# Optimization experiments

Measured on AMD Instinct MI355X. Metric: run time of the kernel, lower is better.

The kernel has to match this reference:

```python
import jax, jax.numpy as jnp
import numpy as np

B, T, C = 4, 2048, 1024
H, D = 16, 64          # n_head, head_size; H*D == C
FF = 4 * C             # compute_layer_scaling * n_embed
EPS = 1e-5


def layernorm(x, g, b):
    mu = jnp.mean(x, axis=-1, keepdims=True)
    var = jnp.var(x, axis=-1, keepdims=True)
    return (x - mu) * jax.lax.rsqrt(var + EPS) * g + b


def setup_inputs() -> dict:
    key = jax.random.key(0)
    ks = jax.random.split(key, 12)
    s_c = 1.0 / np.sqrt(C)
    s_ff = 1.0 / np.sqrt(FF)
    return {
        "x": jax.random.normal(ks[0], (B, T, C), dtype=jnp.float32),
        # per-head Q/K/V weights, stacked: [H, C, D] (Linear with bias=False)
        "Wq": jax.random.normal(ks[1], (H, C, D), dtype=jnp.float32) * s_c,
        "Wk": jax.random.normal(ks[2], (H, C, D), dtype=jnp.float32) * s_c,
        "Wv": jax.random.normal(ks[3], (H, C, D), dtype=jnp.float32) * s_c,
        "Wproj": jax.random.normal(ks[4], (C, C), dtype=jnp.float32) * s_c,
        "bproj": jnp.zeros((C,), dtype=jnp.float32),
        "W1": jax.random.normal(ks[5], (C, FF), dtype=jnp.float32) * s_c,
        "b1": jnp.zeros((FF,), dtype=jnp.float32),
        "W2": jax.random.normal(ks[6], (FF, FF), dtype=jnp.float32) * s_ff,
        "b2": jnp.zeros((FF,), dtype=jnp.float32),
        "W3": jax.random.normal(ks[7], (FF, C), dtype=jnp.float32) * s_ff,
        "b3": jnp.zeros((C,), dtype=jnp.float32),
        "ln1_g": jnp.ones((C,), dtype=jnp.float32),
        "ln1_b": jnp.zeros((C,), dtype=jnp.float32),
        "ln2_g": jnp.ones((C,), dtype=jnp.float32),
        "ln2_b": jnp.zeros((C,), dtype=jnp.float32),
    }


def reference(x, Wq, Wk, Wv, Wproj, bproj, W1, b1, W2, b2, W3, b3,
              ln1_g, ln1_b, ln2_g, ln2_b):
    # --- multi-head causal self-attention (pre-LN) ---
    h = layernorm(x, ln1_g, ln1_b)
    q = jnp.einsum("btc,hcd->bhtd", h, Wq)
    k = jnp.einsum("btc,hcd->bhtd", h, Wk)
    v = jnp.einsum("btc,hcd->bhtd", h, Wv)
    # NOTE: original scales by n_embed**-0.5 (C from x.shape), not head_size
    scores = jnp.einsum("bhtd,bhsd->bhts", q, k) * (C ** -0.5)
    causal = jnp.tril(jnp.ones((T, T), dtype=bool))
    scores = jnp.where(causal, scores, -jnp.inf)
    wei = jax.nn.softmax(scores, axis=-1)          # dropout p=0 -> identity
    attn = jnp.einsum("bhts,bhsd->bhtd", wei, v)
    attn = attn.transpose(0, 2, 1, 3).reshape(B, T, C)  # concat heads
    x = x + attn @ Wproj + bproj
    # --- feed-forward (pre-LN): C -> FF -> relu -> FF -> relu -> C ---
    h2 = layernorm(x, ln2_g, ln2_b)
    h2 = jax.nn.relu(h2 @ W1 + b1)
    h2 = jax.nn.relu(h2 @ W2 + b2)
    x = x + h2 @ W3 + b3
    return x
```

## Files before the change

kernel.cpp:

```cpp
#include <hip/hip_runtime.h>

typedef __bf16 bf16;
typedef bf16  bf16x8 __attribute__((ext_vector_type(8)));
typedef bf16  bf16x4 __attribute__((ext_vector_type(4)));
typedef float f32x4  __attribute__((ext_vector_type(4)));

#define T_SEQ 2048

__device__ __forceinline__ void gload_lds16(const bf16* g, bf16* l) {
    __builtin_amdgcn_global_load_lds(
        (const __attribute__((address_space(1))) unsigned int*)g,
        (__attribute__((address_space(3))) unsigned int*)l,
        16, 0, 0);
}

#define VMCNT(n) asm volatile("s_waitcnt vmcnt(" #n ")" ::: "memory")
#define BAR() do { asm volatile("" ::: "memory"); __builtin_amdgcn_s_barrier(); \
                   asm volatile("" ::: "memory"); } while (0)

__global__ __launch_bounds__(256) void transpose_f32_bf16(
    const float* __restrict__ in, bf16* __restrict__ out, int R, int Cc, int ldo)
{
    __shared__ float tile[32][33];
    const int bx = blockIdx.x * 32;
    const int by = blockIdx.y * 32;
    const long bi = (long)blockIdx.z * R * Cc;
    const long bo = (long)blockIdx.z * Cc * ldo;
    const int tx = threadIdx.x, ty = threadIdx.y;
#pragma unroll
    for (int i = 0; i < 4; ++i)
        tile[ty + i * 8][tx] = in[bi + (long)(by + ty + i * 8) * Cc + bx + tx];
    __syncthreads();
#pragma unroll
    for (int i = 0; i < 4; ++i)
        out[bo + (long)(bx + ty + i * 8) * ldo + by + tx] = (bf16)tile[tx][ty + i * 8];
}

__global__ __launch_bounds__(256) void transpose_bf16(
    const bf16* __restrict__ in, bf16* __restrict__ out, int ldi, int ldo)
{
    __shared__ bf16 tile[32][33];
    const int bx = blockIdx.x * 32;
    const int by = blockIdx.y * 32;
    const int tx = threadIdx.x, ty = threadIdx.y;
#pragma unroll
    for (int i = 0; i < 4; ++i)
        tile[ty + i * 8][tx] = in[(long)(by + ty + i * 8) * ldi + bx + tx];
    __syncthreads();
#pragma unroll
    for (int i = 0; i < 4; ++i)
        out[(long)(bx + ty + i * 8) * ldo + by + tx] = tile[tx][ty + i * 8];
}

__global__ __launch_bounds__(256) void ln_kernel(
    const float* __restrict__ x, const float* __restrict__ g,
    const float* __restrict__ bb, bf16* __restrict__ out)
{
    const long row = blockIdx.x;
    const int tid = threadIdx.x;
    const float4 v = ((const float4*)(x + row * 1024))[tid];
    float s  = v.x + v.y + v.z + v.w;
    float s2 = v.x * v.x + v.y * v.y + v.z * v.z + v.w * v.w;
#pragma unroll
    for (int off = 32; off >= 1; off >>= 1) {
        s  += __shfl_xor(s,  off, 64);
        s2 += __shfl_xor(s2, off, 64);
    }
    __shared__ float red[8];
    const int wid = tid >> 6;
    if ((tid & 63) == 0) { red[wid] = s; red[4 + wid] = s2; }
    __syncthreads();
    s  = red[0] + red[1] + red[2] + red[3];
    s2 = red[4] + red[5] + red[6] + red[7];
    const float mu   = s * (1.f / 1024.f);
    const float rstd = rsqrtf(s2 * (1.f / 1024.f) - mu * mu + 1e-5f);
    const float4 gv = ((const float4*)g)[tid];
    const float4 bv = ((const float4*)bb)[tid];
    bf16x4 ov;
    ov[0] = (bf16)((v.x - mu) * rstd * gv.x + bv.x);
    ov[1] = (bf16)((v.y - mu) * rstd * gv.y + bv.y);
    ov[2] = (bf16)((v.z - mu) * rstd * gv.z + bv.z);
    ov[3] = (bf16)((v.w - mu) * rstd * gv.w + bv.w);
    *(bf16x4*)(out + row * 1024 + tid * 4) = ov;
}

#define LOADA(BUFP, QM) do {                                                   \
    const char* ab_ = (BUFP) + (size_t)((wr * 64 + (QM) * 128 + fr) * 128);    \
    _Pragma("unroll") for (int m_ = 0; m_ < 4; ++m_) {                         \
        af[m_][0] = *(const bf16x8*)(ab_ + m_ * 2048 + so0);                   \
        af[m_][1] = *(const bf16x8*)(ab_ + m_ * 2048 + so1); } } while (0)

#define LOADB(BUFP, QN) do {                                                   \
    const char* bb_ = (BUFP) + (size_t)((wc * 32 + (QN) * 128 + fr) * 128);    \
    _Pragma("unroll") for (int n_ = 0; n_ < 2; ++n_) {                         \
        bfv[n_][0] = *(const bf16x8*)(bb_ + n_ * 2048 + so0);                  \
        bfv[n_][1] = *(const bf16x8*)(bb_ + n_ * 2048 + so1); } } while (0)

#define MMA(ACC) do { __builtin_amdgcn_s_setprio(1);                           \
    _Pragma("unroll") for (int m_ = 0; m_ < 4; ++m_)                           \
    _Pragma("unroll") for (int n_ = 0; n_ < 2; ++n_) {                         \
        ACC[m_][n_] = __builtin_amdgcn_mfma_f32_16x16x32_bf16(                 \
            af[m_][0], bfv[n_][0], ACC[m_][n_], 0, 0, 0);                      \
        ACC[m_][n_] = __builtin_amdgcn_mfma_f32_16x16x32_bf16(                 \
            af[m_][1], bfv[n_][1], ACC[m_][n_], 0, 0, 0); }                    \
    __builtin_amdgcn_s_setprio(0); } while (0)

#define TILE_BODY(PRE) do {                                                    \
    const char* abuf = cAs + ((size_t)cur << 15);                              \
    const char* bbuf = cBs + ((size_t)cur << 15);                              \
    const long kn = (long)(k + 1) * 64;                                        \
    LOADA(abuf, 0);                                                            \
    LOADB(bbuf, 0);                                                            \
    if (PRE) { stageA(nxt, 0, kn); stageB(nxt, 0, kn);                         \
               stageB(nxt, 1, kn); stageA(nxt, 1, kn); VMCNT(10); }            \
    else     { VMCNT(2); }                                                     \
    BAR(); MMA(a00); BAR();                                                    \
    LOADB(bbuf, 1);                                                            \
    if (PRE) { VMCNT(8); } else { VMCNT(0); }                                  \
    BAR(); MMA(a01); BAR();                                                    \
    LOADA(abuf, 1);                                                            \
    BAR(); MMA(a11); BAR();                                                    \
    LOADB(bbuf, 0);                                                            \
    if (PRE) { VMCNT(4); }                                                     \
    BAR(); MMA(a10); BAR(); } while (0)

template <int MODE>
__global__ __launch_bounds__(512, 2) void gemm256(
    const bf16* __restrict__ A, const bf16* __restrict__ Bt,
    const float* __restrict__ bias, const float* __restrict__ resid,
    void* __restrict__ outp, int M, int N, int K, int nbn)
{
    extern __shared__ __align__(16) char smem[];
    char* cAs = smem;
    char* cBs = smem + 65536;

    const int tid = threadIdx.x;
    const int wid = tid >> 6, lane = tid & 63;
    const int wr = wid >> 2, wc = wid & 3;
    const int fr = lane & 15, fq = lane >> 4;

    const int nwg = gridDim.x;
    const int cpx = nwg >> 3;
    const int b0  = blockIdx.x;
    const int bid = (b0 & 7) * cpx + (b0 >> 3);
    const long bm = bid / nbn, bn = bid % nbn;
    const long bmrow = bm * 256, bnrow = bn * 256;

    const int srow0 = wid * 8 + (lane >> 3);
    const int sslot = (lane & 7) ^ (lane >> 3);
    auto stageA = [&](int buf, int h, long kt) {
        const bf16* g = A + (size_t)(bmrow + h * 128 + srow0) * K + kt + sslot * 8;
        char* l = cAs + ((size_t)buf << 15) + h * 16384 + (size_t)wid * 1024;
        gload_lds16(g, (bf16*)l);
        gload_lds16(g + (size_t)64 * K, (bf16*)(l + 8192));
    };
    auto stageB = [&](int buf, int h, long kt) {
        const bf16* g = Bt + (size_t)(bnrow + h * 128 + srow0) * K + kt + sslot * 8;
        char* l = cBs + ((size_t)buf << 15) + h * 16384 + (size_t)wid * 1024;
        gload_lds16(g, (bf16*)l);
        gload_lds16(g + (size_t)64 * K, (bf16*)(l + 8192));
    };

    const int sx  = fr & 7;
    const int so0 = ((fq) ^ sx) * 16;
    const int so1 = ((4 + fq) ^ sx) * 16;

    bf16x8 af[4][2], bfv[2][2];
    f32x4 a00[4][2], a01[4][2], a11[4][2], a10[4][2];
#pragma unroll
    for (int m = 0; m < 4; ++m)
#pragma unroll
        for (int n = 0; n < 2; ++n) {
            a00[m][n] = {0.f, 0.f, 0.f, 0.f}; a01[m][n] = {0.f, 0.f, 0.f, 0.f};
            a11[m][n] = {0.f, 0.f, 0.f, 0.f}; a10[m][n] = {0.f, 0.f, 0.f, 0.f};
        }

    stageA(0, 0, 0); stageB(0, 0, 0); stageB(0, 1, 0); stageA(0, 1, 0);
    VMCNT(4);
    BAR();

    const int NT = K >> 6;
    int cur = 0, nxt = 1;
    int k = 0;
    for (; k < NT - 1; ++k) {
        cur = k & 1; nxt = cur ^ 1;
        TILE_BODY(true);
    }
    cur = k & 1; nxt = cur ^ 1;
    TILE_BODY(false);

    auto writeQ = [&](f32x4 (&acc)[4][2], int QM, int QN) {
#pragma unroll
        for (int m = 0; m < 4; ++m) {
            const long row0 = bmrow + wr * 64 + QM * 128 + m * 16 + fq * 4;
#pragma unroll
            for (int n = 0; n < 2; ++n) {
                const long col = bnrow + wc * 32 + QN * 128 + n * 16 + fr;
                const float bv = (MODE == 0) ? 0.f : bias[col];
#pragma unroll
                for (int j = 0; j < 4; ++j) {
                    const long row = row0 + j;
                    float v = acc[m][n][j] + bv;
                    if (MODE == 1) v = fmaxf(v, 0.f);
                    if (MODE == 2) {
                        v += resid[row * N + col];
                        ((float*)outp)[row * N + col] = v;
                    } else {
                        ((bf16*)outp)[row * N + col] = (bf16)v;
                    }
                }
            }
        }
    };
    writeQ(a00, 0, 0); writeQ(a01, 0, 1); writeQ(a11, 1, 1); writeQ(a10, 1, 0);
}

#define TILE_BODY_N(PRE, LAST) do {                                            \
    const char* abuf = cAs + ((size_t)cur << 15);                              \
    const char* bbuf = cBs + ((size_t)cur << 14);                              \
    const long kn = (long)(k + 1) * 64;                                        \
    LOADA(abuf, 0);                                                            \
    LOADB(bbuf, 0);                                                            \
    if (PRE) { stageA(nxt, 0, kn); stageB(nxt, kn); stageA(nxt, 1, kn);        \
               VMCNT(6); }                                                     \
    else     { VMCNT(0); }                                                     \
    BAR(); MMA(aq0); BAR();                                                    \
    LOADA(abuf, 1);                                                            \
    if (PRE) { VMCNT(2); }                                                     \
    if (!LAST) { BAR(); }                                                      \
    MMA(aq1);                                                                  \
    if (!LAST) { BAR(); } } while (0)

template <int MODE>
__global__ __launch_bounds__(512, 2) void gemm256n(
    const bf16* __restrict__ A, const bf16* __restrict__ Bt,
    const float* __restrict__ bias, const float* __restrict__ resid,
    void* __restrict__ outp, int M, int N, int K, int nbn)
{
    extern __shared__ __align__(16) char smem[];
    char* cAs = smem;
    char* cBs = smem + 65536;

    const int tid = threadIdx.x;
    const int wid = tid >> 6, lane = tid & 63;
    const int wr = wid >> 2, wc = wid & 3;
    const int fr = lane & 15, fq = lane >> 4;

    const int nwg = gridDim.x;
    const int cpx = nwg >> 3;
    const int b0  = blockIdx.x;
    const int bid = (b0 & 7) * cpx + (b0 >> 3);
    const long bm = bid / nbn, bn = bid % nbn;
    const long bmrow = bm * 256, bnrow = bn * 128;

    const int srow0 = wid * 8 + (lane >> 3);
    const int sslot = (lane & 7) ^ (lane >> 3);
    auto stageA = [&](int buf, int h, long kt) {
        const bf16* g = A + (size_t)(bmrow + h * 128 + srow0) * K + kt + sslot * 8;
        char* l = cAs + ((size_t)buf << 15) + h * 16384 + (size_t)wid * 1024;
        gload_lds16(g, (bf16*)l);
        gload_lds16(g + (size_t)64 * K, (bf16*)(l + 8192));
    };
    auto stageB = [&](int buf, long kt) {
        const bf16* g = Bt + (size_t)(bnrow + srow0) * K + kt + sslot * 8;
        char* l = cBs + ((size_t)buf << 14) + (size_t)wid * 1024;
        gload_lds16(g, (bf16*)l);
        gload_lds16(g + (size_t)64 * K, (bf16*)(l + 8192));
    };

    const int sx  = fr & 7;
    const int so0 = ((fq) ^ sx) * 16;
    const int so1 = ((4 + fq) ^ sx) * 16;

    bf16x8 af[4][2], bfv[2][2];
    f32x4 aq0[4][2], aq1[4][2];
#pragma unroll
    for (int m = 0; m < 4; ++m)
#pragma unroll
        for (int n = 0; n < 2; ++n) {
            aq0[m][n] = {0.f, 0.f, 0.f, 0.f};
            aq1[m][n] = {0.f, 0.f, 0.f, 0.f};
        }

    stageA(0, 0, 0); stageB(0, 0); stageA(0, 1, 0);
    VMCNT(2);
    BAR();

    const int NT = K >> 6;
    int cur = 0, nxt = 1;
    int k = 0;
    for (; k < NT - 1; ++k) {
        cur = k & 1; nxt = cur ^ 1;
        TILE_BODY_N(true, false);
    }
    cur = k & 1; nxt = cur ^ 1;
    TILE_BODY_N(false, true);

    auto writeQ = [&](f32x4 (&acc)[4][2], int QM) {
#pragma unroll
        for (int m = 0; m < 4; ++m) {
            const long row0 = bmrow + wr * 64 + QM * 128 + m * 16 + fq * 4;
#pragma unroll
            for (int n = 0; n < 2; ++n) {
                const long col = bnrow + wc * 32 + n * 16 + fr;
                const float bv = (MODE == 0) ? 0.f : bias[col];
#pragma unroll
                for (int j = 0; j < 4; ++j) {
                    const long row = row0 + j;
                    float v = acc[m][n][j] + bv;
                    if (MODE == 1) v = fmaxf(v, 0.f);
                    if (MODE == 2) {
                        v += resid[row * N + col];
                        ((float*)outp)[row * N + col] = v;
                    } else {
                        ((bf16*)outp)[row * N + col] = (bf16)v;
                    }
                }
            }
        }
    };
    writeQ(aq0, 0); writeQ(aq1, 1);
}

__device__ __forceinline__ void attn_step(
    const bf16* __restrict__ Ks, const bf16* __restrict__ Vt,
    bf16* __restrict__ Pp, const bf16x8* qf,
    f32x4* o, f32x4& o_l, float* mj, const bf16x8 onesf,
    int fr, int fq, int qloc, bool diag)
{
    f32x4 s[4];
#pragma unroll
    for (int n = 0; n < 4; ++n) s[n] = {0.f, 0.f, 0.f, 0.f};
#pragma unroll
    for (int n = 0; n < 4; ++n) {
        const int t  = n * 16 + fr;
        const int sw = ((t ^ (t >> 3)) & 7) << 4;
#pragma unroll
        for (int kk = 0; kk < 2; ++kk) {
            const bf16x8 kf = *(const bf16x8*)((const char*)Ks + t * 128
                                               + ((kk * 64 + fq * 16) ^ sw));
            s[n] = __builtin_amdgcn_mfma_f32_16x16x32_bf16(qf[kk], kf, s[n], 0, 0, 0);
        }
    }
    float v[4][4], mxj[4];
#pragma unroll
    for (int j = 0; j < 4; ++j) {
        const int qg = qloc + fq * 4 + j;
        v[0][j] = s[0][j] * 0.03125f;
        v[1][j] = s[1][j] * 0.03125f;
        v[2][j] = s[2][j] * 0.03125f;
        v[3][j] = s[3][j] * 0.03125f;
        if (diag) {
            if (fr      > qg) v[0][j] = -1e30f;
            if (16 + fr > qg) v[1][j] = -1e30f;
            if (32 + fr > qg) v[2][j] = -1e30f;
            if (48 + fr > qg) v[3][j] = -1e30f;
        }
        float mx = fmaxf(fmaxf(v[0][j], v[1][j]), fmaxf(v[2][j], v[3][j]));
#pragma unroll
        for (int off = 1; off <= 8; off <<= 1) mx = fmaxf(mx, __shfl_xor(mx, off, 16));
        mxj[j] = mx;
    }
    float need = mxj[0] - mj[0];
    need = fmaxf(need, mxj[1] - mj[1]);
    need = fmaxf(need, mxj[2] - mj[2]);
    need = fmaxf(need, mxj[3] - mj[3]);
    if (__any(need > 8.f)) {
#pragma unroll
        for (int j = 0; j < 4; ++j) {
            const float mn   = fmaxf(mj[j], mxj[j]);
            const float corr = __expf(mj[j] - mn);
            mj[j] = mn;
#pragma unroll
            for (int nd = 0; nd < 4; ++nd) o[nd][j] *= corr;
            o_l[j] *= corr;
        }
    }
#pragma unroll
    for (int j = 0; j < 4; ++j) {
        bf16* prow = Pp + (fq * 4 + j) * 72;
        prow[fr]      = (bf16)__expf(v[0][j] - mj[j]);
        prow[16 + fr] = (bf16)__expf(v[1][j] - mj[j]);
        prow[32 + fr] = (bf16)__expf(v[2][j] - mj[j]);
        prow[48 + fr] = (bf16)__expf(v[3][j] - mj[j]);
    }
    asm volatile("s_waitcnt lgkmcnt(0)" ::: "memory");
    __builtin_amdgcn_sched_barrier(0);
    const bf16x8 pf0 = *(const bf16x8*)(Pp + fr * 72 + fq * 8);
    const bf16x8 pf1 = *(const bf16x8*)(Pp + fr * 72 + 32 + fq * 8);
#pragma unroll
    for (int nd = 0; nd < 4; ++nd) {
        const int dd = nd * 16 + fr;
        const int sw = ((dd ^ (dd >> 3)) & 7) << 4;
        const bf16x8 vf0 = *(const bf16x8*)((const char*)Vt + dd * 128 + ((fq * 16) ^ sw));
        const bf16x8 vf1 = *(const bf16x8*)((const char*)Vt + dd * 128 + ((64 + fq * 16) ^ sw));
        o[nd] = __builtin_amdgcn_mfma_f32_16x16x32_bf16(pf0, vf0, o[nd], 0, 0, 0);
        o[nd] = __builtin_amdgcn_mfma_f32_16x16x32_bf16(pf1, vf1, o[nd], 0, 0, 0);
    }
    o_l = __builtin_amdgcn_mfma_f32_16x16x32_bf16(pf0, onesf, o_l, 0, 0, 0);
    o_l = __builtin_amdgcn_mfma_f32_16x16x32_bf16(pf1, onesf, o_l, 0, 0, 0);
}

__global__ __launch_bounds__(256) void attn_kernel(
    const bf16* __restrict__ qkv, const bf16* __restrict__ vt,
    bf16* __restrict__ out)
{
    const int pair = blockIdx.x;
    const int h = blockIdx.y, b = blockIdx.z;
    const int tid = threadIdx.x, wid = tid >> 6, lane = tid & 63;
    const int fr = lane & 15, fq = lane >> 4;
    const int jA = pair, jB = 31 - pair;
    const bf16* baseQ = qkv + ((long)b * T_SEQ) * 3072 + h * 64;
    const bf16* baseK = baseQ + 1024;
    const bf16* baseV = vt + (long)(h * 64) * 8192 + (long)b * T_SEQ;

    __shared__ __align__(16) bf16 Ks[2][64 * 64];
    __shared__ __align__(16) bf16 Vs[2][64 * 64];
    __shared__ __align__(16) bf16 Plds[4][16 * 72];

    const int qrA = jA * 64 + wid * 16 + fr;
    const int qrB = jB * 64 + wid * 16 + fr;
    bf16x8 qfA[2], qfB[2];
#pragma unroll
    for (int kk = 0; kk < 2; ++kk) {
        qfA[kk] = *(const bf16x8*)(baseQ + (long)qrA * 3072 + kk * 32 + fq * 8);
        qfB[kk] = *(const bf16x8*)(baseQ + (long)qrB * 3072 + kk * 32 + fq * 8);
    }

    bf16x8 onesf;
    {
        const bf16 ov = (fr == 0) ? (bf16)1.f : (bf16)0.f;
#pragma unroll
        for (int e = 0; e < 8; ++e) onesf[e] = ov;
    }

    f32x4 oA[4], oB[4], olA, olB;
    float mA[4], mB[4];
#pragma unroll
    for (int nd = 0; nd < 4; ++nd) { oA[nd] = {0.f, 0.f, 0.f, 0.f}; oB[nd] = {0.f, 0.f, 0.f, 0.f}; }
    olA = {0.f, 0.f, 0.f, 0.f}; olB = {0.f, 0.f, 0.f, 0.f};
#pragma unroll
    for (int j = 0; j < 4; ++j) { mA[j] = -1e30f; mB[j] = -1e30f; }

    const int t_p0 = wid * 16 + (lane >> 3);
    const int t_p1 = t_p0 + 8;
    const int kcb0 = ((lane & 7) * 16) ^ (((t_p0 ^ (t_p0 >> 3)) & 7) << 4);
    const int kcb1 = ((lane & 7) * 16) ^ (((t_p1 ^ (t_p1 >> 3)) & 7) << 4);

    bf16* P = &Plds[wid][0];

    auto stage = [&](int buf, int c) {
        const long s0 = (long)c * 64;
        gload_lds16(baseK + (s0 + t_p0) * 3072 + (kcb0 >> 1), &Ks[buf][(wid * 2) * 512]);
        gload_lds16(baseK + (s0 + t_p1) * 3072 + (kcb1 >> 1), &Ks[buf][(wid * 2 + 1) * 512]);
        gload_lds16(baseV + (long)t_p0 * 8192 + s0 + (kcb0 >> 1), &Vs[buf][(wid * 2) * 512]);
        gload_lds16(baseV + (long)t_p1 * 8192 + s0 + (kcb1 >> 1), &Vs[buf][(wid * 2 + 1) * 512]);
    };

    const int nch = jB + 1;
    stage(0, 0);
    for (int c = 0; c < nch; ++c) {
        const int cur = c & 1;
        if (c + 1 < nch) { stage(cur ^ 1, c + 1); VMCNT(4); }
        else             { VMCNT(0); }
        BAR();
        if (c <= jA)
            attn_step(Ks[cur], Vs[cur], P, qfA, oA, olA, mA, onesf, fr, fq, wid * 16, c == jA);
        attn_step(Ks[cur], Vs[cur], P, qfB, oB, olB, mB, onesf, fr, fq, wid * 16, c == jB);
        BAR();
    }

#pragma unroll
    for (int j = 0; j < 4; ++j) {
        const float lA = __shfl(olA[j], lane & 48, 64);
        const float lB = __shfl(olB[j], lane & 48, 64);
        const float rA = 1.f / lA, rB = 1.f / lB;
        const long rowA = (long)b * T_SEQ + jA * 64 + wid * 16 + fq * 4 + j;
        const long rowB = (long)b * T_SEQ + jB * 64 + wid * 16 + fq * 4 + j;
#pragma unroll
        for (int nd = 0; nd < 4; ++nd) {
            out[rowA * 1024 + h * 64 + nd * 16 + fr] = (bf16)(oA[nd][j] * rA);
            out[rowB * 1024 + h * 64 + nd * 16 + fr] = (bf16)(oB[nd][j] * rB);
        }
    }
}

extern "C" void kernel_launch(void* const* d_in, const int* in_sizes, int n_in,
                              void* d_out, int out_size, void* d_ws, size_t ws_size,
                              hipStream_t stream)
{
    const float* x     = (const float*)d_in[0];
    const float* Wq    = (const float*)d_in[1];
    const float* Wk    = (const float*)d_in[2];
    const float* Wv    = (const float*)d_in[3];
    const float* Wproj = (const float*)d_in[4];
    const float* bproj = (const float*)d_in[5];
    const float* W1    = (const float*)d_in[6];
    const float* b1    = (const float*)d_in[7];
    const float* W2    = (const float*)d_in[8];
    const float* b2    = (const float*)d_in[9];
    const float* W3    = (const float*)d_in[10];
    const float* b3    = (const float*)d_in[11];
    const float* ln1g  = (const float*)d_in[12];
    const float* ln1b  = (const float*)d_in[13];
    const float* ln2g  = (const float*)d_in[14];
    const float* ln2b  = (const float*)d_in[15];

    char* ws = (char*)d_ws;
    size_t off = 0;
    auto alloc = [&](size_t bytes) {
        void* p = ws + off;
        off += (bytes + 255) & ~(size_t)255;
        return p;
    };
    bf16* Wqkv_t  = (bf16*)alloc(3072ul * 1024 * 2);
    bf16* Wproj_t = (bf16*)alloc(1024ul * 1024 * 2);
    bf16* W1_t    = (bf16*)alloc(4096ul * 1024 * 2);
    bf16* W2_t    = (bf16*)alloc(4096ul * 4096 * 2);
    bf16* W3_t    = (bf16*)alloc(1024ul * 4096 * 2);
    bf16* hbuf    = (bf16*)alloc(8192ul * 1024 * 2);
    float* x1     = (float*)alloc(8192ul * 1024 * 4);
    bf16* a1      = (bf16*)alloc(8192ul * 4096 * 2);
    char* R1      = (char*)alloc(8192ul * 4096 * 2);
    bf16* qkvb    = (bf16*)R1;
    bf16* attnb   = (bf16*)(R1 + 8192ul * 3072 * 2);
    bf16* a2      = (bf16*)R1;
    bf16* vt      = a1;

    hipFuncSetAttribute(reinterpret_cast<const void*>(&gemm256<1>),
                        hipFuncAttributeMaxDynamicSharedMemorySize, 131072);
    hipFuncSetAttribute(reinterpret_cast<const void*>(&gemm256n<0>),
                        hipFuncAttributeMaxDynamicSharedMemorySize, 98304);
    hipFuncSetAttribute(reinterpret_cast<const void*>(&gemm256n<2>),
                        hipFuncAttributeMaxDynamicSharedMemorySize, 98304);

    const dim3 tb(32, 8);
    transpose_f32_bf16<<<dim3(2, 32, 16), tb, 0, stream>>>(Wq, Wqkv_t,                1024, 64, 1024);
    transpose_f32_bf16<<<dim3(2, 32, 16), tb, 0, stream>>>(Wk, Wqkv_t + 1024l * 1024, 1024, 64, 1024);
    transpose_f32_bf16<<<dim3(2, 32, 16), tb, 0, stream>>>(Wv, Wqkv_t + 2048l * 1024, 1024, 64, 1024);
    transpose_f32_bf16<<<dim3(32, 32, 1),   tb, 0, stream>>>(Wproj, Wproj_t, 1024, 1024, 1024);
    transpose_f32_bf16<<<dim3(128, 32, 1),  tb, 0, stream>>>(W1, W1_t, 1024, 4096, 1024);
    transpose_f32_bf16<<<dim3(128, 128, 1), tb, 0, stream>>>(W2, W2_t, 4096, 4096, 4096);
    transpose_f32_bf16<<<dim3(32, 128, 1),  tb, 0, stream>>>(W3, W3_t, 4096, 1024, 4096);

    ln_kernel<<<8192, 256, 0, stream>>>(x, ln1g, ln1b, hbuf);
    gemm256n<0><<<768, 512, 98304, stream>>>(hbuf, Wqkv_t, nullptr, nullptr, qkvb,
                                             8192, 3072, 1024, 24);
    transpose_bf16<<<dim3(32, 256), tb, 0, stream>>>(qkvb + 2048, vt, 3072, 8192);
    attn_kernel<<<dim3(16, 16, 4), 256, 0, stream>>>(qkvb, vt, attnb);
    gemm256n<2><<<256, 512, 98304, stream>>>(attnb, Wproj_t, bproj, x, x1,
                                             8192, 1024, 1024, 8);
    ln_kernel<<<8192, 256, 0, stream>>>(x1, ln2g, ln2b, hbuf);
    gemm256<1><<<512, 512, 131072, stream>>>(hbuf, W1_t, b1, nullptr, a1,
                                             8192, 4096, 1024, 16);
    gemm256<1><<<512, 512, 131072, stream>>>(a1, W2_t, b2, nullptr, a2,
                                             8192, 4096, 4096, 16);
    gemm256n<2><<<256, 512, 98304, stream>>>(a2, W3_t, b3, x1, (float*)d_out,
                                             8192, 1024, 4096, 8);
}
```

Measured before the change: 717.8 us.

## Deepen GEMM global-to-LDS prefetch pipeline by spreading stages across subtiles

Restructures the GEMM main loop so global_load_lds staging of the next tiles is interleaved across the four MMA quadrants, and starts loading quadrants of tile k+2 into the current buffer once those quadrants are consumed. The prologue prefetches part of the second tile, and vmcnt waits are retuned for the deeper pipeline. The goal is to hide more global memory latency behind MFMA work. It adds tricky buffer-reuse ordering that could introduce races if the wait counts are wrong.

```diff
diff --git a/kernel.cpp b/kernel.cpp
--- a/kernel.cpp
+++ b/kernel.cpp
@@ -105,23 +105,25 @@
             af[m_][1], bfv[n_][1], ACC[m_][n_], 0, 0, 0); }                    \
     __builtin_amdgcn_s_setprio(0); } while (0)
 
-#define TILE_BODY(PRE) do {                                                    \
+#define TB_DEEP(W1N, W3N, ISSN, ISSC) do {                                     \
     const char* abuf = cAs + ((size_t)cur << 15);                              \
     const char* bbuf = cBs + ((size_t)cur << 15);                              \
-    const long kn = (long)(k + 1) * 64;                                        \
+    const long kb  = (long)(k + 1) * 64;                                       \
+    const long kb2 = (long)(k + 2) * 64;                                       \
     LOADA(abuf, 0);                                                            \
     LOADB(bbuf, 0);                                                            \
-    if (PRE) { stageA(nxt, 0, kn); stageB(nxt, 0, kn);                         \
-               stageB(nxt, 1, kn); stageA(nxt, 1, kn); VMCNT(10); }            \
-    else     { VMCNT(2); }                                                     \
+    if (ISSN) stageB(nxt, 0, kb);                                 \
     BAR(); MMA(a00); BAR();                                                    \
     LOADB(bbuf, 1);                                                            \
-    if (PRE) { VMCNT(8); } else { VMCNT(0); }                                  \
+    if (ISSN) stageA(nxt, 1, kb);                                 \
+    VMCNT(W1N);                                                                \
     BAR(); MMA(a01); BAR();                                                    \
     LOADA(abuf, 1);                                                            \
+    if (ISSC) stageA(cur, 0, kb2);                                \
     BAR(); MMA(a11); BAR();                                                    \
     LOADB(bbuf, 0);                                                            \
-    if (PRE) { VMCNT(4); }                                                     \
+    if (ISSC) stageB(cur, 1, kb2);                                \
+    VMCNT(W3N);                                                                \
     BAR(); MMA(a10); BAR(); } while (0)
 
 template <int MODE>
@@ -175,19 +177,27 @@
             a11[m][n] = {0.f, 0.f, 0.f, 0.f}; a10[m][n] = {0.f, 0.f, 0.f, 0.f};
         }
 
-    stageA(0, 0, 0); stageB(0, 0, 0); stageB(0, 1, 0); stageA(0, 1, 0);
-    VMCNT(4);
+    stageA(0, 0, 0);
+    stageB(0, 1, 0);
+    stageB(0, 0, 0);
+    stageA(0, 1, 0);
+    stageA(1, 0, 64);
+    stageB(1, 1, 64);
+    VMCNT(6);
     BAR();
 
     const int NT = K >> 6;
-    int cur = 0, nxt = 1;
+    int cur, nxt;
     int k = 0;
-    for (; k < NT - 1; ++k) {
+    for (; k < NT - 2; ++k) {
         cur = k & 1; nxt = cur ^ 1;
-        TILE_BODY(true);
+        TB_DEEP(8, 6, true, true);
     }
     cur = k & 1; nxt = cur ^ 1;
-    TILE_BODY(false);
+    TB_DEEP(8, 2, true, false);
+    ++k;
+    cur = k & 1; nxt = cur ^ 1;
+    TB_DEEP(0, 0, false, false);
 
     auto writeQ = [&](f32x4 (&acc)[4][2], int QM, int QN) {
 #pragma unroll
```

Measured after the change: 683.4 us. 1.05x faster.
